# Kernel optimization log

Hardware: AMD Instinct MI355X
Metric: run time of the kernel (lower is better)

Reference implementation:

```python
import jax, jax.numpy as jnp
import numpy as np

MARGIN = 0.3
EPS = 1e-12


def setup_inputs() -> dict:
    key = jax.random.key(0)
    k1, k2 = jax.random.split(key)
    n, d = 4096, 1024
    inputs = jax.random.normal(k1, (n, d), dtype=jnp.float32)
    targets = jax.random.randint(k2, (n,), 0, 64, dtype=jnp.int64)
    return {"inputs": inputs, "targets": targets}


def reference(inputs, targets):
    n = inputs.shape[0]
    # pairwise Euclidean distance matrix: ||xi||^2 + ||xj||^2 - 2 xi.xj
    sq = jnp.sum(inputs * inputs, axis=1)  # [n]
    dist2 = sq[:, None] + sq[None, :] - 2.0 * (inputs @ inputs.T)
    dist = jnp.sqrt(jnp.clip(dist2, EPS))  # [n, n]
    # same-label mask (includes diagonal, matching original)
    mask = targets[:, None] == targets[None, :]
    # fused masked row-wise hard mining
    neg_inf = jnp.asarray(-jnp.inf, dist.dtype)
    pos_inf = jnp.asarray(jnp.inf, dist.dtype)
    dist_ap = jnp.max(jnp.where(mask, dist, neg_inf), axis=1)  # hardest positive
    dist_an = jnp.min(jnp.where(mask, pos_inf, dist), axis=1)  # hardest negative
    # MarginRankingLoss with y=1: mean(relu(margin - (dist_an - dist_ap)))
    loss = jnp.mean(jnp.maximum(MARGIN - (dist_an - dist_ap), 0.0))
    prec = jnp.sum((dist_an > dist_ap).astype(jnp.float32)) / n
    return (loss, prec)
```

## Files before the change

### kernel.cpp

```cpp
#include <hip/hip_runtime.h>
#include <stdint.h>

#define MARGIN 0.3f
#define EPS 1e-12f

typedef __attribute__((ext_vector_type(8))) __bf16 bf16x8;
typedef __attribute__((ext_vector_type(4))) float f32x4;

__device__ __forceinline__ unsigned short f2bf(float f) {
    unsigned u = __float_as_uint(f);
    unsigned r = (u + 0x7FFFu + ((u >> 16) & 1u)) >> 16;
    return (unsigned short)r;
}

#define GLD16(gp, lp)                                                     \
    __builtin_amdgcn_global_load_lds(                                     \
        (const __attribute__((address_space(1))) void*)(gp),              \
        (__attribute__((address_space(3))) void*)(lp), 16, 0, 0)

__global__ __launch_bounds__(256) void prep_kernel(
    const float* __restrict__ X, unsigned short* __restrict__ Xbf,
    float* __restrict__ sqg, unsigned* __restrict__ apb,
    unsigned* __restrict__ anb, unsigned* __restrict__ ctr, int d) {
    const int wave = threadIdx.x >> 6, lane = threadIdx.x & 63;
    const int row = blockIdx.x * 4 + wave;
    const float4* Xr = (const float4*)(X + (size_t)row * d);
    ushort4* Or = (ushort4*)(Xbf + (size_t)row * d);
    float s = 0.0f;
    const int nq = d >> 2;
    for (int i = lane; i < nq; i += 64) {
        float4 v = Xr[i];
        s += v.x * v.x + v.y * v.y + v.z * v.z + v.w * v.w;
        ushort4 o;
        o.x = f2bf(v.x); o.y = f2bf(v.y); o.z = f2bf(v.z); o.w = f2bf(v.w);
        Or[i] = o;
    }
    for (int off = 32; off > 0; off >>= 1) s += __shfl_down(s, off, 64);
    if (lane == 0) {
        sqg[row] = s;
        apb[row] = 0u;
        anb[row] = 0x7F800000u;
    }
    if (blockIdx.x == 0 && threadIdx.x == 0) ctr[0] = 0u;
}

#define BM 256
#define BN 256
#define BK 64

__global__ __launch_bounds__(512, 2) void gram_gemm(
    const unsigned short* __restrict__ Xbf, const float* __restrict__ sqg,
    const int* __restrict__ tgt, unsigned* __restrict__ apb,
    unsigned* __restrict__ anb, unsigned* __restrict__ ctr,
    float* __restrict__ out, int n, int d, int nblk) {
    __shared__ unsigned short ldsA[2][BM * BK];
    __shared__ unsigned short ldsB[2][BN * BK];

    const int tid  = threadIdx.x;
    const int lane = tid & 63;
    const int wave = tid >> 6;
    const int wm = wave >> 2;
    const int wn = wave & 3;
    const int lo = lane & 15, hi = lane >> 4;

    const int orig = blockIdx.x;
    const int bid = (orig & 7) * 32 + (orig >> 3);
    const int bi = bid >> 4, bj = bid & 15;
    const int rowBase = bi * BM;
    const int colBase = bj * BN;

    const int srow = lane >> 3;
    const int sk   = (((lane & 7) ^ srow) * 8);
    const unsigned short* gA[4];
    const unsigned short* gB[4];
#pragma unroll
    for (int c = 0; c < 4; ++c) {
        const int rr = wave * 32 + c * 8 + srow;
        gA[c] = Xbf + (size_t)(rowBase + rr) * d + sk;
        gB[c] = Xbf + (size_t)(colBase + rr) * d + sk;
    }

#define STAGE(bufi, k0)                                                   \
    do {                                                                  \
        _Pragma("unroll")                                                 \
        for (int c = 0; c < 4; ++c) {                                     \
            GLD16(gA[c] + (k0), &ldsA[bufi][(wave * 32 + c * 8) * BK]);   \
            GLD16(gB[c] + (k0), &ldsB[bufi][(wave * 32 + c * 8) * BK]);   \
        }                                                                 \
    } while (0)

    f32x4 acc[8][4] = {};

    const int nt = d / BK;
    int cur = 0;
    STAGE(0, 0);
    __syncthreads();

    for (int t = 0; t < nt; ++t) {
        if (t + 1 < nt) STAGE(cur ^ 1, (t + 1) * BK);
#pragma unroll
        for (int kk = 0; kk < 2; ++kk) {
            bf16x8 a[8], b[4];
            const int slot = ((kk * 4 + hi) ^ (lo & 7)) * 8;
#pragma unroll
            for (int mi = 0; mi < 8; ++mi)
                a[mi] = *(const bf16x8*)
                    &ldsA[cur][(wm * 128 + mi * 16 + lo) * BK + slot];
#pragma unroll
            for (int ni = 0; ni < 4; ++ni)
                b[ni] = *(const bf16x8*)
                    &ldsB[cur][(wn * 64 + ni * 16 + lo) * BK + slot];
            __builtin_amdgcn_s_setprio(1);
#pragma unroll
            for (int mi = 0; mi < 8; ++mi)
#pragma unroll
                for (int ni = 0; ni < 4; ++ni)
                    acc[mi][ni] = __builtin_amdgcn_mfma_f32_16x16x32_bf16(
                        a[mi], b[ni], acc[mi][ni], 0, 0, 0);
            __builtin_amdgcn_s_setprio(0);
        }
        __syncthreads();
        cur ^= 1;
    }

    float sqj[4];
    int   tj[4];
#pragma unroll
    for (int ni = 0; ni < 4; ++ni) {
        const int gj = colBase + wn * 64 + ni * 16 + lo;
        sqj[ni] = sqg[gj];
        tj[ni]  = tgt[gj];
    }
#pragma unroll
    for (int mi = 0; mi < 8; ++mi) {
#pragma unroll
        for (int j = 0; j < 4; ++j) {
            const int gi = rowBase + wm * 128 + mi * 16 + hi * 4 + j;
            const float sqi = sqg[gi];
            const int   ti  = tgt[gi];
            float ap = 0.0f;
            float an = __uint_as_float(0x7F800000u);
#pragma unroll
            for (int ni = 0; ni < 4; ++ni) {
                const float d2 = sqi + sqj[ni] - 2.0f * acc[mi][ni][j];
                const float dist = sqrtf(fmaxf(d2, EPS));
                if (ti == tj[ni]) ap = fmaxf(ap, dist);
                else              an = fminf(an, dist);
            }
#pragma unroll
            for (int m = 1; m < 16; m <<= 1) {
                ap = fmaxf(ap, __shfl_xor(ap, m, 64));
                an = fminf(an, __shfl_xor(an, m, 64));
            }
            if (lo == 0) {
                atomicMax(&apb[gi], __float_as_uint(ap));
                atomicMin(&anb[gi], __float_as_uint(an));
            }
        }
    }

    __threadfence();
    __syncthreads();
    __shared__ int lastFlag;
    if (tid == 0) {
        unsigned prev = __hip_atomic_fetch_add(ctr, 1u, __ATOMIC_ACQ_REL,
                                               __HIP_MEMORY_SCOPE_AGENT);
        lastFlag = (prev == (unsigned)(nblk - 1)) ? 1 : 0;
    }
    __syncthreads();
    if (lastFlag) {
        float ls = 0.0f, pc = 0.0f;
        for (int i = tid; i < n; i += 512) {
            const float ap = __uint_as_float(__hip_atomic_load(
                &apb[i], __ATOMIC_RELAXED, __HIP_MEMORY_SCOPE_AGENT));
            const float an = __uint_as_float(__hip_atomic_load(
                &anb[i], __ATOMIC_RELAXED, __HIP_MEMORY_SCOPE_AGENT));
            ls += fmaxf(MARGIN - (an - ap), 0.0f);
            pc += (an > ap) ? 1.0f : 0.0f;
        }
        __shared__ float rl[8], rp[8];
        for (int off = 32; off > 0; off >>= 1) {
            ls += __shfl_down(ls, off, 64);
            pc += __shfl_down(pc, off, 64);
        }
        if ((tid & 63) == 0) { rl[tid >> 6] = ls; rp[tid >> 6] = pc; }
        __syncthreads();
        if (tid == 0) {
            float L = 0.0f, P = 0.0f;
#pragma unroll
            for (int w = 0; w < 8; ++w) { L += rl[w]; P += rp[w]; }
            out[0] = L / (float)n;
            out[1] = P / (float)n;
        }
    }
}

__global__ __launch_bounds__(256) void fb_zero(float* __restrict__ out) {
    if (threadIdx.x == 0) { out[0] = 0.0f; out[1] = 0.0f; }
}

__global__ __launch_bounds__(256) void fb_row(
    const float* __restrict__ X, const int* __restrict__ tgt,
    float* __restrict__ out, int n, int d) {
    __shared__ float xi[4096];
    const int i = blockIdx.x;
    const int tid = threadIdx.x;
    for (int k = tid; k < d; k += 256) xi[k] = X[(size_t)i * d + k];
    __syncthreads();
    const int ti = tgt[i];
    float ap = 0.0f;
    float an = __uint_as_float(0x7F800000u);
    for (int j = tid; j < n; j += 256) {
        const float4* Xj = (const float4*)(X + (size_t)j * d);
        float s = 0.0f;
        for (int k4 = 0; k4 < (d >> 2); ++k4) {
            float4 v = Xj[k4];
            float4 u = *(const float4*)&xi[k4 * 4];
            float dx = u.x - v.x, dy = u.y - v.y, dz = u.z - v.z, dw = u.w - v.w;
            s += dx * dx + dy * dy + dz * dz + dw * dw;
        }
        const float dist = sqrtf(fmaxf(s, EPS));
        if (tgt[j] == ti) ap = fmaxf(ap, dist);
        else              an = fminf(an, dist);
    }
    for (int m = 1; m < 64; m <<= 1) {
        ap = fmaxf(ap, __shfl_xor(ap, m, 64));
        an = fminf(an, __shfl_xor(an, m, 64));
    }
    __shared__ float rap[4], ran[4];
    const int wave = tid >> 6, lane = tid & 63;
    if (lane == 0) { rap[wave] = ap; ran[wave] = an; }
    __syncthreads();
    if (tid == 0) {
        ap = fmaxf(fmaxf(rap[0], rap[1]), fmaxf(rap[2], rap[3]));
        an = fminf(fminf(ran[0], ran[1]), fminf(ran[2], ran[3]));
        atomicAdd(&out[0], fmaxf(MARGIN - (an - ap), 0.0f));
        atomicAdd(&out[1], (an > ap) ? 1.0f : 0.0f);
    }
}

__global__ __launch_bounds__(64) void fb_scale(float* __restrict__ out, float inv_n) {
    if (threadIdx.x == 0) { out[0] *= inv_n; out[1] *= inv_n; }
}

extern "C" void kernel_launch(void* const* d_in, const int* in_sizes, int n_in,
                              void* d_out, int out_size, void* d_ws, size_t ws_size,
                              hipStream_t stream) {
    const float* X   = (const float*)d_in[0];
    const int*   tgt = (const int*)d_in[1];
    const int n = in_sizes[1];
    const int d = in_sizes[0] / n;

    const size_t need = (size_t)n * d * 2 + (size_t)n * 4 * 3 + 4;
    if (ws_size >= need && (n % BM) == 0 && (d % BK) == 0 &&
        ((n / BM) % 8 == 0 || (n / BM) * (n / BM) % 8 == 0)) {
        char* ws = (char*)d_ws;
        unsigned short* Xbf = (unsigned short*)ws;
        float*    sqg = (float*)(ws + (size_t)n * d * 2);
        unsigned* apb = (unsigned*)((char*)sqg + (size_t)n * 4);
        unsigned* anb = apb + n;
        unsigned* ctr = anb + n;

        const int nb = n / BM;
        const int nblk = nb * nb;
        prep_kernel<<<n / 4, 256, 0, stream>>>(X, Xbf, sqg, apb, anb, ctr, d);
        gram_gemm<<<nblk, 512, 0, stream>>>(Xbf, sqg, tgt, apb, anb, ctr,
                                            (float*)d_out, n, d, nblk);
    } else {
        fb_zero<<<1, 256, 0, stream>>>((float*)d_out);
        fb_row<<<n, 256, 0, stream>>>(X, tgt, (float*)d_out, n, d);
        fb_scale<<<1, 64, 0, stream>>>((float*)d_out, 1.0f / (float)n);
    }
}
```

Baseline: 154.2 us.

## Interleave half-tile global-to-LDS staging with MFMA phases in GEMM main loop

Restructures the bf16 Gram GEMM main loop so that each K-tile is split into four MFMA phases, each followed by issuing part of the next tile's global_load_lds and a raw s_barrier. Explicit vmcnt waits replace the full __syncthreads per tile. The aim is to spread memory issue across compute and cut synchronization stalls, in the style of a ping-pong schedule. The cost is more complex hand-managed barriers and waitcnts, with a risk of LDS races. The dispatch condition is also tightened to require d divisible by 2*BK.

Measured after the change: 149.9 us. 2.8% less time.

```diff
diff --git a/kernel.cpp b/kernel.cpp
--- a/kernel.cpp
+++ b/kernel.cpp
@@ -71,56 +71,129 @@
 
     const int srow = lane >> 3;
     const int sk   = (((lane & 7) ^ srow) * 8);
-    const unsigned short* gA[4];
-    const unsigned short* gB[4];
-#pragma unroll
-    for (int c = 0; c < 4; ++c) {
-        const int rr = wave * 32 + c * 8 + srow;
-        gA[c] = Xbf + (size_t)(rowBase + rr) * d + sk;
-        gB[c] = Xbf + (size_t)(colBase + rr) * d + sk;
-    }
-
-#define STAGE(bufi, k0)                                                   \
-    do {                                                                  \
-        _Pragma("unroll")                                                 \
-        for (int c = 0; c < 4; ++c) {                                     \
-            GLD16(gA[c] + (k0), &ldsA[bufi][(wave * 32 + c * 8) * BK]);   \
-            GLD16(gB[c] + (k0), &ldsB[bufi][(wave * 32 + c * 8) * BK]);   \
-        }                                                                 \
-    } while (0)
+    const unsigned short* gA[2][2];
+    const unsigned short* gB[2][2];
+    int dA[2][2], dB[2][2];
+#pragma unroll
+    for (int h = 0; h < 2; ++h)
+#pragma unroll
+        for (int c = 0; c < 2; ++c) {
+            const int rr = h * 128 + wave * 16 + c * 8;
+            gA[h][c] = Xbf + (size_t)(rowBase + rr + srow) * d + sk;
+            gB[h][c] = Xbf + (size_t)(colBase + rr + srow) * d + sk;
+            dA[h][c] = rr * BK;
+            dB[h][c] = rr * BK;
+        }
+
+#define STG_A(buf, h, k0)                                                  \
+    do { GLD16(gA[h][0] + (k0), &ldsA[buf][dA[h][0]]);                     \
+         GLD16(gA[h][1] + (k0), &ldsA[buf][dA[h][1]]); } while (0)
+#define STG_B(buf, h, k0)                                                  \
+    do { GLD16(gB[h][0] + (k0), &ldsB[buf][dB[h][0]]);                     \
+         GLD16(gB[h][1] + (k0), &ldsB[buf][dB[h][1]]); } while (0)
 
     f32x4 acc[8][4] = {};
-
     const int nt = d / BK;
-    int cur = 0;
-    STAGE(0, 0);
-    __syncthreads();
-
-    for (int t = 0; t < nt; ++t) {
-        if (t + 1 < nt) STAGE(cur ^ 1, (t + 1) * BK);
-#pragma unroll
-        for (int kk = 0; kk < 2; ++kk) {
-            bf16x8 a[8], b[4];
-            const int slot = ((kk * 4 + hi) ^ (lo & 7)) * 8;
-#pragma unroll
-            for (int mi = 0; mi < 8; ++mi)
-                a[mi] = *(const bf16x8*)
-                    &ldsA[cur][(wm * 128 + mi * 16 + lo) * BK + slot];
-#pragma unroll
-            for (int ni = 0; ni < 4; ++ni)
-                b[ni] = *(const bf16x8*)
-                    &ldsB[cur][(wn * 64 + ni * 16 + lo) * BK + slot];
-            __builtin_amdgcn_s_setprio(1);
-#pragma unroll
-            for (int mi = 0; mi < 8; ++mi)
-#pragma unroll
-                for (int ni = 0; ni < 4; ++ni)
-                    acc[mi][ni] = __builtin_amdgcn_mfma_f32_16x16x32_bf16(
-                        a[mi], b[ni], acc[mi][ni], 0, 0, 0);
-            __builtin_amdgcn_s_setprio(0);
-        }
-        __syncthreads();
-        cur ^= 1;
+    const int sl0 = (hi ^ (lo & 7)) * 8;
+    const int sl1 = ((4 + hi) ^ (lo & 7)) * 8;
+
+    STG_B(0, 0, 0);
+    STG_B(0, 1, 0);
+    STG_A(0, 0, 0);
+    STG_A(0, 1, 0);
+    STG_B(1, 0, BK);
+
+    bf16x8 a[4], b0[4], b1[4];
+
+    for (int T = 0; T < nt - 1; ++T) {
+        const int cb = T & 1, nbuf = cb ^ 1;
+        const int kn = (T + 1) * BK;
+        STG_B(nbuf, 1, kn);
+        asm volatile("s_waitcnt vmcnt(4)" ::: "memory");
+        asm volatile("s_barrier" ::: "memory");
+#pragma unroll
+        for (int mi = 0; mi < 4; ++mi)
+            a[mi] = *(const bf16x8*)&ldsA[cb][(wm * 128 + mi * 16 + lo) * BK + sl0];
+#pragma unroll
+        for (int ni = 0; ni < 4; ++ni)
+            b0[ni] = *(const bf16x8*)&ldsB[cb][(wn * 64 + ni * 16 + lo) * BK + sl0];
+        __builtin_amdgcn_s_setprio(1);
+#pragma unroll
+        for (int mi = 0; mi < 4; ++mi)
+#pragma unroll
+            for (int ni = 0; ni < 4; ++ni)
+                acc[mi][ni] = __builtin_amdgcn_mfma_f32_16x16x32_bf16(
+                    a[mi], b0[ni], acc[mi][ni], 0, 0, 0);
+        __builtin_amdgcn_s_setprio(0);
+        STG_A(nbuf, 0, kn);
+        asm volatile("s_barrier" ::: "memory");
+#pragma unroll
+        for (int mi = 0; mi < 4; ++mi)
+            a[mi] = *(const bf16x8*)&ldsA[cb][(wm * 128 + (mi + 4) * 16 + lo) * BK + sl0];
+        __builtin_amdgcn_s_setprio(1);
+#pragma unroll
+        for (int mi = 0; mi < 4; ++mi)
+#pragma unroll
+            for (int ni = 0; ni < 4; ++ni)
+                acc[mi + 4][ni] = __builtin_amdgcn_mfma_f32_16x16x32_bf16(
+                    a[mi], b0[ni], acc[mi + 4][ni], 0, 0, 0);
+        __builtin_amdgcn_s_setprio(0);
+        STG_A(nbuf, 1, kn);
+        asm volatile("s_barrier" ::: "memory");
+#pragma unroll
+        for (int mi = 0; mi < 4; ++mi)
+            a[mi] = *(const bf16x8*)&ldsA[cb][(wm * 128 + mi * 16 + lo) * BK + sl1];
+#pragma unroll
+        for (int ni = 0; ni < 4; ++ni)
+            b1[ni] = *(const bf16x8*)&ldsB[cb][(wn * 64 + ni * 16 + lo) * BK + sl1];
+        __builtin_amdgcn_s_setprio(1);
+#pragma unroll
+        for (int mi = 0; mi < 4; ++mi)
+#pragma unroll
+            for (int ni = 0; ni < 4; ++ni)
+                acc[mi][ni] = __builtin_amdgcn_mfma_f32_16x16x32_bf16(
+                    a[mi], b1[ni], acc[mi][ni], 0, 0, 0);
+        __builtin_amdgcn_s_setprio(0);
+        asm volatile("s_barrier" ::: "memory");
+        if (T < nt - 2) STG_B(cb, 0, kn + BK);
+#pragma unroll
+        for (int mi = 0; mi < 4; ++mi)
+            a[mi] = *(const bf16x8*)&ldsA[cb][(wm * 128 + (mi + 4) * 16 + lo) * BK + sl1];
+        __builtin_amdgcn_s_setprio(1);
+#pragma unroll
+        for (int mi = 0; mi < 4; ++mi)
+#pragma unroll
+            for (int ni = 0; ni < 4; ++ni)
+                acc[mi + 4][ni] = __builtin_amdgcn_mfma_f32_16x16x32_bf16(
+                    a[mi], b1[ni], acc[mi + 4][ni], 0, 0, 0);
+        __builtin_amdgcn_s_setprio(0);
+    }
+    {
+        const int cb = (nt - 1) & 1;
+        asm volatile("s_waitcnt vmcnt(0)" ::: "memory");
+        asm volatile("s_barrier" ::: "memory");
+#pragma unroll
+        for (int half = 0; half < 2; ++half) {
+            const int sl = half ? sl1 : sl0;
+#pragma unroll
+            for (int ni = 0; ni < 4; ++ni)
+                b0[ni] = *(const bf16x8*)&ldsB[cb][(wn * 64 + ni * 16 + lo) * BK + sl];
+#pragma unroll
+            for (int mh = 0; mh < 2; ++mh) {
+#pragma unroll
+                for (int mi = 0; mi < 4; ++mi)
+                    a[mi] = *(const bf16x8*)
+                        &ldsA[cb][(wm * 128 + (mi + mh * 4) * 16 + lo) * BK + sl];
+                __builtin_amdgcn_s_setprio(1);
+#pragma unroll
+                for (int mi = 0; mi < 4; ++mi)
+#pragma unroll
+                    for (int ni = 0; ni < 4; ++ni)
+                        acc[mi + mh * 4][ni] = __builtin_amdgcn_mfma_f32_16x16x32_bf16(
+                            a[mi], b0[ni], acc[mi + mh * 4][ni], 0, 0, 0);
+                __builtin_amdgcn_s_setprio(0);
+            }
+        }
     }
 
     float sqj[4];
@@ -252,8 +325,8 @@
     const int d = in_sizes[0] / n;
 
     const size_t need = (size_t)n * d * 2 + (size_t)n * 4 * 3 + 4;
-    if (ws_size >= need && (n % BM) == 0 && (d % BK) == 0 &&
-        ((n / BM) % 8 == 0 || (n / BM) * (n / BM) % 8 == 0)) {
+    if (ws_size >= need && (n % BM) == 0 && (d % (2 * BK)) == 0 &&
+        ((n / BM) * (n / BM)) % 8 == 0) {
         char* ws = (char*)d_ws;
         unsigned short* Xbf = (unsigned short*)ws;
         float*    sqg = (float*)(ws + (size_t)n * d * 2);
```
